# Kernel tuning notes

Measured on AMD Instinct MI355X. Metric: run time of the kernel, lower is better.

Reference implementation:

```python
import jax, jax.numpy as jnp
import numpy as np

EPS = 1e-12  # torch F.normalize eps


def setup_inputs() -> dict:
    key = jax.random.key(0)
    k1, k2, k3 = jax.random.split(key, 3)
    B, way, shot, D, H, W = 64, 5, 1, 640, 5, 5
    nq = 75
    base = jax.random.normal(k1, (B, way, shot, D, H, W), dtype=jnp.float32)
    query = jax.random.normal(k2, (B, nq, D, H, W), dtype=jnp.float32)
    r = jax.random.normal(k3, (2,), dtype=jnp.float32) * 0.1
    return {"base": base, "query": query, "r": r, "neighbor_k": 5}


def reference(base, query, r, neighbor_k):
    B, way, shot, D, H, W = base.shape
    nq = query.shape[1]
    hw = H * W

    # ---- global-cosine branch: spatial-mean descriptors ----
    base_mean = base.reshape(B, way * shot, D, hw).mean(axis=-1)   # [B, way*shot, D]
    query_mean = query.reshape(B, nq, D, hw).mean(axis=-1)         # [B, nq, D]
    bm = base_mean / jnp.maximum(jnp.linalg.norm(base_mean, axis=-1, keepdims=True), EPS)
    qm = query_mean / jnp.maximum(jnp.linalg.norm(query_mean, axis=-1, keepdims=True), EPS)
    logits = jnp.einsum('bqd,bkd->bqk', qm, bm)                    # [B, nq, way*shot]

    # ---- DN4 image-to-class branch (vectorized over the original triple loop) ----
    # query local descriptors: [B, nq, hw, D], L2-normalized over channels
    q = query.reshape(B, nq, D, hw).transpose(0, 1, 3, 2)
    q = q / jnp.linalg.norm(q, axis=-1, keepdims=True)
    # support local descriptors: base_mix [B, way, shot*D, hw], column-normalized
    s = base.reshape(B, way, shot * D, hw)
    s = s / jnp.linalg.norm(s, axis=2, keepdims=True)
    # cosine sims between every query patch and every support patch of each class
    # (requires shot*D == D, i.e. shot == 1, as in the original code)
    sim = jnp.einsum('bqpd,bkdl->bqkpl', q, s)                     # [B, nq, way, hw, hw]
    topk_vals, _ = jax.lax.top_k(sim, neighbor_k)                  # [B, nq, way, hw, k]
    logits_dn4 = topk_vals.sum(axis=(-1, -2)) / neighbor_k         # [B, nq, way]

    return r[0] * logits + r[1] * logits_dn4
```

## Files before the change

### kernel.cpp

```cpp
#include <hip/hip_runtime.h>
#include <hip/hip_bf16.h>
#include <math.h>

#define NB    64
#define WAY   5
#define DCH   640
#define HW    25
#define NQ    75
#define NBK   5
#define EPSN  1e-12f

#define QPB   4
#define BPB   ((NQ + QPB - 1) / QPB)
#define NWK   (NB * BPB)
#define NDG   (DCH / 8)
#define SCOLS 128
#define CD    32
#define NCHK  (DCH / CD)
#define CFL   (CD * HW)

typedef __attribute__((ext_vector_type(8)))  short  bf16x8;
typedef __attribute__((ext_vector_type(8)))  ushort u16x8;
typedef __attribute__((ext_vector_type(16))) float  f32x16;
typedef __attribute__((ext_vector_type(4)))  float  f32x4;

#define AS1 __attribute__((address_space(1)))
#define AS3 __attribute__((address_space(3)))

__device__ inline ushort f2bf(float f) {
    uint u = __float_as_uint(f);
    return (ushort)((u + 0x7FFFu + ((u >> 16) & 1u)) >> 16);
}

__global__ __launch_bounds__(256) void k_prep(const float* __restrict__ base,
                                              float* __restrict__ invs,
                                              float* __restrict__ invsm,
                                              ushort* __restrict__ sT)
{
    const int bk = blockIdx.x;
    const int b  = bk / WAY;
    const int k  = bk - b * WAY;
    const float* src = base + (size_t)bk * (DCH * HW);
    __shared__ float lds[DCH * HW];
    __shared__ float red[256];
    const int tid = threadIdx.x;

    const f32x4* s4 = (const f32x4*)src;
    f32x4* l4 = (f32x4*)lds;
    for (int i = tid; i < (DCH * HW) / 4; i += 256)
        l4[i] = __builtin_nontemporal_load(s4 + i);
    __syncthreads();

    if (tid < HW) {
        float ss = 0.f;
        for (int d = 0; d < DCH; ++d) { float v = lds[d * HW + tid]; ss = fmaf(v, v, ss); }
        invs[bk * HW + tid] = rsqrtf(ss);
    }

    float ssq = 0.f;
    for (int d = tid; d < DCH; d += 256) {
        float s = 0.f;
        #pragma unroll
        for (int pp = 0; pp < HW; ++pp) s += lds[d * HW + pp];
        float m = s * (1.0f / HW);
        ssq = fmaf(m, m, ssq);
    }
    red[tid] = ssq;
    __syncthreads();
    for (int s = 128; s > 0; s >>= 1) {
        if (tid < s) red[tid] += red[tid + s];
        __syncthreads();
    }
    if (tid == 0) invsm[bk] = 1.0f / fmaxf(sqrtf(red[0]), EPSN);

    ushort* dstb = sT + (size_t)b * (NDG * SCOLS * 8);
    for (int t = tid; t < NDG * HW; t += 256) {
        const int dg = t / HW, l = t - dg * HW;
        u16x8 v;
        #pragma unroll
        for (int e = 0; e < 8; ++e) v[e] = f2bf(lds[(dg * 8 + e) * HW + l]);
        *(u16x8*)&dstb[((size_t)dg * SCOLS + k * HW + l) * 8] = v;
    }
    if (k == 0) {
        const u16x8 z = (u16x8)(ushort)0;
        for (int t = tid; t < NDG * 3; t += 256) {
            const int dg = t / 3, sc = 125 + (t - dg * 3);
            *(u16x8*)&dstb[((size_t)dg * SCOLS + sc) * 8] = z;
        }
    }
}

__global__ __launch_bounds__(256, 2) void k_fused(const float* __restrict__ query,
                                                  const ushort* __restrict__ sT,
                                                  const float* __restrict__ invs,
                                                  const float* __restrict__ invsm,
                                                  const float* __restrict__ r,
                                                  float* __restrict__ out)
{
    __shared__ __align__(16) float lds_q[QPB][2][CFL];
    __shared__ float invs_l[SCOLS];
    __shared__ float invsm_l[WAY];

    const int tid  = threadIdx.x;
    const int wid  = tid >> 6;
    const int lane = tid & 63;
    const int p    = lane & 31;
    const int hi   = lane >> 5;

    const int wk = (blockIdx.x & 7) * (int)(gridDim.x >> 3) + (blockIdx.x >> 3);
    const int b  = wk / BPB;
    const int qb = wk - b * BPB;
    const int q  = qb * QPB + wid;
    const bool qok = q < NQ;

    if (tid < WAY * HW) invs_l[tid] = invs[b * WAY * HW + tid];
    if (tid >= WAY * HW && tid < SCOLS) invs_l[tid] = 0.f;
    if (tid < WAY)      invsm_l[tid] = invsm[b * WAY + tid];
    __syncthreads();
    if (!qok) return;

    f32x16 acc0 = {}, acc1 = {}, acc2 = {}, acc3 = {}, accg = {};

    const int pc = (p < HW) ? p : (HW - 1);
    const float* qrow = query + (size_t)(b * NQ + q) * (DCH * HW);
    const ushort* sTb = sT + (size_t)b * (NDG * SCOLS * 8);

#define ISSUE(c)                                                               \
    {                                                                          \
        const float* src_ = qrow + (c) * CFL;                                  \
        float* dst_ = &lds_q[wid][(c) & 1][0];                                 \
        _Pragma("unroll")                                                      \
        for (int i = 0; i < 3; ++i)                                            \
            __builtin_amdgcn_global_load_lds(                                  \
                (const AS1 uint*)(src_ + i * 256 + lane * 4),                  \
                (AS3 uint*)(dst_ + i * 256), 16, 0, 0);                        \
        if (lane < 8)                                                          \
            __builtin_amdgcn_global_load_lds(                                  \
                (const AS1 uint*)(src_ + 768 + lane * 4),                      \
                (AS3 uint*)(dst_ + 768), 16, 0, 0);                            \
    }

#define LOAD_AF(BANK, c)                                                       \
    {                                                                          \
        _Pragma("unroll")                                                      \
        for (int ks = 0; ks < 2; ++ks) {                                       \
            const int dg = (c) * 4 + ks * 2 + hi;                              \
            const bf16x8* arow = (const bf16x8*)(sTb + (size_t)dg * SCOLS * 8);\
            BANK[ks * 4 + 0] = arow[p];                                        \
            BANK[ks * 4 + 1] = arow[32 + p];                                   \
            BANK[ks * 4 + 2] = arow[64 + p];                                   \
            BANK[ks * 4 + 3] = arow[96 + p];                                   \
        }                                                                      \
    }

#define COMPUTE(c, BANK)                                                       \
    {                                                                          \
        __builtin_amdgcn_s_setprio(1);                                         \
        const float* qb_lds = &lds_q[wid][(c) & 1][hi * 8 * HW + pc];          \
        _Pragma("unroll")                                                      \
        for (int ks = 0; ks < 2; ++ks) {                                       \
            const float v0 = qb_lds[(ks * 16 + 0) * HW];                       \
            const float v1 = qb_lds[(ks * 16 + 1) * HW];                       \
            const float v2 = qb_lds[(ks * 16 + 2) * HW];                       \
            const float v3 = qb_lds[(ks * 16 + 3) * HW];                       \
            const float v4 = qb_lds[(ks * 16 + 4) * HW];                       \
            const float v5 = qb_lds[(ks * 16 + 5) * HW];                       \
            const float v6 = qb_lds[(ks * 16 + 6) * HW];                       \
            const float v7 = qb_lds[(ks * 16 + 7) * HW];                       \
            union { uint u[4]; bf16x8 v; } bqu;                                \
            asm("v_cvt_pk_bf16_f32 %0, %1, %2" : "=v"(bqu.u[0]) : "v"(v0), "v"(v1)); \
            asm("v_cvt_pk_bf16_f32 %0, %1, %2" : "=v"(bqu.u[1]) : "v"(v2), "v"(v3)); \
            asm("v_cvt_pk_bf16_f32 %0, %1, %2" : "=v"(bqu.u[2]) : "v"(v4), "v"(v5)); \
            asm("v_cvt_pk_bf16_f32 %0, %1, %2" : "=v"(bqu.u[3]) : "v"(v6), "v"(v7)); \
            const bf16x8 bq = bqu.v;                                           \
            acc0 = __builtin_amdgcn_mfma_f32_32x32x16_bf16(BANK[ks * 4 + 0], bq, acc0, 0, 0, 0); \
            acc1 = __builtin_amdgcn_mfma_f32_32x32x16_bf16(BANK[ks * 4 + 1], bq, acc1, 0, 0, 0); \
            acc2 = __builtin_amdgcn_mfma_f32_32x32x16_bf16(BANK[ks * 4 + 2], bq, acc2, 0, 0, 0); \
            acc3 = __builtin_amdgcn_mfma_f32_32x32x16_bf16(BANK[ks * 4 + 3], bq, acc3, 0, 0, 0); \
            accg = __builtin_amdgcn_mfma_f32_32x32x16_bf16(bq, bq, accg, 0, 0, 0); \
        }                                                                      \
        __builtin_amdgcn_s_setprio(0);                                         \
    }

#define STEP(c, CUR, NXT)                                                      \
    {                                                                          \
        if ((c) + 1 < NCHK) {                                                  \
            asm volatile("s_waitcnt lgkmcnt(0)" ::: "memory");                 \
            ISSUE((c) + 1)                                                     \
            LOAD_AF(NXT, (c) + 1)                                              \
            asm volatile("s_waitcnt vmcnt(12)" ::: "memory");                  \
        } else {                                                               \
            asm volatile("s_waitcnt vmcnt(0)" ::: "memory");                   \
        }                                                                      \
        __builtin_amdgcn_sched_barrier(0);                                     \
        COMPUTE(c, CUR)                                                        \
    }

    bf16x8 afA[8], afB[8];
    ISSUE(0)
    LOAD_AF(afA, 0)

    #pragma unroll 1
    for (int c = 0; c < NCHK; c += 2) {
        STEP(c,     afA, afB)
        STEP(c + 1, afB, afA)
    }
#undef ISSUE
#undef LOAD_AF
#undef COMPUTE
#undef STEP

    const bool pok = p < HW;

    float diag = 0.f, qq = 0.f;
    #pragma unroll
    for (int rr = 0; rr < 16; ++rr) {
        const int rowb = (rr & 3) + 8 * (rr >> 2);
        const int row  = rowb + 4 * hi;
        diag = (row == p) ? accg[rr] : diag;
        if (row < HW && pok) qq += accg[rr];
    }
    diag += __shfl_xor(diag, 32);
    const float invq = rsqrtf(diag);

    float gs[WAY] = {0.f, 0.f, 0.f, 0.f, 0.f};
#define TILE_SUM(ACC, T)                                            \
    _Pragma("unroll")                                               \
    for (int rr = 0; rr < 16; ++rr) {                               \
        const int s0 = (T) * 32 + (rr & 3) + 8 * (rr >> 2);         \
        const float v0 = (hi || !pok) ? 0.f : ACC[rr];              \
        const float v1 = (hi && pok) ? ACC[rr] : 0.f;               \
        if (s0 < 125)     gs[s0 / 25]       += v0;                  \
        if (s0 + 4 < 125) gs[(s0 + 4) / 25] += v1;                  \
    }
    TILE_SUM(acc0, 0) TILE_SUM(acc1, 1) TILE_SUM(acc2, 2) TILE_SUM(acc3, 3)
#undef TILE_SUM

    #pragma unroll
    for (int o = 1; o < 64; o <<= 1) {
        qq += __shfl_xor(qq, o);
        #pragma unroll
        for (int g = 0; g < WAY; ++g) gs[g] += __shfl_xor(gs[g], o);
    }

#define SCALE(ACC, T)                                               \
    _Pragma("unroll")                                               \
    for (int rr = 0; rr < 16; ++rr) {                               \
        const int s0 = (T) * 32 + (rr & 3) + 8 * (rr >> 2);         \
        ACC[rr] *= invs_l[s0 + 4 * hi];                             \
    }
    SCALE(acc0, 0) SCALE(acc1, 1) SCALE(acc2, 2) SCALE(acc3, 3)
#undef SCALE

    float tots[WAY];
    #pragma unroll
    for (int g = 0; g < WAY; ++g) {
        float t0 = -3.402823466e38f, t1 = t0, t2 = t0, t3 = t0, t4 = t0;
        #pragma unroll
        for (int j = 0; j < HW; ++j) {
            const int scol = g * HW + j;
            const int t = scol >> 5, row = scol & 31;
            const int hreq = (row >> 2) & 1;
            const int rr = (row & 3) | ((row >> 3) << 2);
            const float av = (t == 0) ? acc0[rr] : (t == 1) ? acc1[rr]
                           : (t == 2) ? acc2[rr] : acc3[rr];
            float mine = (hi == hreq) ? av : 0.f;
            mine += __shfl_xor(mine, 32);
            float x = mine, a;
            a = fmaxf(t0, x); x = fminf(t0, x); t0 = a;
            a = fmaxf(t1, x); x = fminf(t1, x); t1 = a;
            a = fmaxf(t2, x); x = fminf(t2, x); t2 = a;
            a = fmaxf(t3, x); x = fminf(t3, x); t3 = a;
            a = fmaxf(t4, x); x = fminf(t4, x); t4 = a;
        }
        tots[g] = pok ? (t0 + t1 + t2 + t3 + t4) * invq : 0.f;
    }
    #pragma unroll
    for (int o = 1; o < 64; o <<= 1) {
        #pragma unroll
        for (int g = 0; g < WAY; ++g) tots[g] += __shfl_xor(tots[g], o);
    }

    const float r0 = r[0], r1 = r[1];
    const float invqm = 1.0f / fmaxf(sqrtf(qq) * (1.0f / HW), EPSN);
    float res[WAY];
    #pragma unroll
    for (int g = 0; g < WAY; ++g)
        res[g] = r0 * gs[g] * (1.0f / 625.0f) * invqm * invsm_l[g]
               + r1 * tots[g] * 0.5f * (1.0f / NBK);

    float ov = res[0];
    ov = (lane == 1) ? res[1] : ov;
    ov = (lane == 2) ? res[2] : ov;
    ov = (lane == 3) ? res[3] : ov;
    ov = (lane == 4) ? res[4] : ov;
    if (lane < WAY) out[(size_t)(b * NQ + q) * WAY + lane] = ov;
}

extern "C" void kernel_launch(void* const* d_in, const int* in_sizes, int n_in,
                              void* d_out, int out_size, void* d_ws, size_t ws_size,
                              hipStream_t stream)
{
    const float* base  = (const float*)d_in[0];
    const float* query = (const float*)d_in[1];
    const float* r     = (const float*)d_in[2];
    float* out = (float*)d_out;

    float* invs   = (float*)d_ws;
    float* invsm  = invs + NB * WAY * HW;
    ushort* sT    = (ushort*)((float*)d_ws + 16384);

    k_prep<<<NB * WAY, 256, 0, stream>>>(base, invs, invsm, sT);
    k_fused<<<NWK, 256, 0, stream>>>(query, sT, invs, invsm, r, out);
}
```

Before: 108.0 us.

## Deepen query LDS prefetch pipeline to four stages with explicit epilogue

Grows the per-wave query staging buffer in LDS from two to four chunk slots and issues global-to-LDS loads three chunks ahead instead of one. The loop is restructured so that support-fragment loads are issued before the LDS-wait, and an explicit tail drains the remaining chunks with decreasing vmcnt thresholds. The aim is to hide global memory latency of the query stream behind MFMA work. In exchange it doubles the query LDS footprint, which may limit occupancy, and makes the vmcnt bookkeeping more fragile.

Result: no change. 108.4 us (+0.3%).

```diff
diff --git a/kernel.cpp b/kernel.cpp
--- a/kernel.cpp
+++ b/kernel.cpp
@@ -97,7 +97,7 @@
                                                   const float* __restrict__ r,
                                                   float* __restrict__ out)
 {
-    __shared__ __align__(16) float lds_q[QPB][2][CFL];
+    __shared__ __align__(16) float lds_q[QPB][4][CFL];
     __shared__ float invs_l[SCOLS];
     __shared__ float invsm_l[WAY];
 
@@ -128,7 +128,7 @@
 #define ISSUE(c)                                                               \
     {                                                                          \
         const float* src_ = qrow + (c) * CFL;                                  \
-        float* dst_ = &lds_q[wid][(c) & 1][0];                                 \
+        float* dst_ = &lds_q[wid][(c) & 3][0];                                 \
         _Pragma("unroll")                                                      \
         for (int i = 0; i < 3; ++i)                                            \
             __builtin_amdgcn_global_load_lds(                                  \
@@ -156,7 +156,7 @@
 #define COMPUTE(c, BANK)                                                       \
     {                                                                          \
         __builtin_amdgcn_s_setprio(1);                                         \
-        const float* qb_lds = &lds_q[wid][(c) & 1][hi * 8 * HW + pc];          \
+        const float* qb_lds = &lds_q[wid][(c) & 3][hi * 8 * HW + pc];          \
         _Pragma("unroll")                                                      \
         for (int ks = 0; ks < 2; ++ks) {                                       \
             const float v0 = qb_lds[(ks * 16 + 0) * HW];                       \
@@ -182,33 +182,48 @@
         __builtin_amdgcn_s_setprio(0);                                         \
     }
 
-#define STEP(c, CUR, NXT)                                                      \
-    {                                                                          \
-        if ((c) + 1 < NCHK) {                                                  \
-            asm volatile("s_waitcnt lgkmcnt(0)" ::: "memory");                 \
-            ISSUE((c) + 1)                                                     \
-            LOAD_AF(NXT, (c) + 1)                                              \
-            asm volatile("s_waitcnt vmcnt(12)" ::: "memory");                  \
-        } else {                                                               \
-            asm volatile("s_waitcnt vmcnt(0)" ::: "memory");                   \
-        }                                                                      \
+#define STEP_SS(c, CUR, NXT)                                                   \
+    {                                                                          \
+        LOAD_AF(NXT, (c) + 1)                                                  \
+        asm volatile("s_waitcnt lgkmcnt(0)" ::: "memory");                     \
+        ISSUE((c) + 3)                                                         \
+        asm volatile("s_waitcnt vmcnt(16)" ::: "memory");                      \
         __builtin_amdgcn_sched_barrier(0);                                     \
         COMPUTE(c, CUR)                                                        \
     }
 
+#define STEP_T(c, CUR, NXT, VMASM)                                             \
+    {                                                                          \
+        LOAD_AF(NXT, (c) + 1)                                                  \
+        asm volatile(VMASM ::: "memory");                                      \
+        __builtin_amdgcn_sched_barrier(0);                                     \
+        COMPUTE(c, CUR)                                                        \
+    }
+
     bf16x8 afA[8], afB[8];
-    ISSUE(0)
+    ISSUE(0) ISSUE(1)
+    __builtin_amdgcn_sched_barrier(0);
     LOAD_AF(afA, 0)
+    __builtin_amdgcn_sched_barrier(0);
+    ISSUE(2)
 
     #pragma unroll 1
-    for (int c = 0; c < NCHK; c += 2) {
-        STEP(c,     afA, afB)
-        STEP(c + 1, afB, afA)
-    }
+    for (int c = 0; c < NCHK - 4; c += 2) {
+        STEP_SS(c,     afA, afB)
+        STEP_SS(c + 1, afB, afA)
+    }
+    STEP_SS(16, afA, afB)
+    STEP_T(17, afB, afA, "s_waitcnt vmcnt(12)")
+    STEP_T(18, afA, afB, "s_waitcnt vmcnt(8)")
+    asm volatile("s_waitcnt vmcnt(0)" ::: "memory");
+    __builtin_amdgcn_sched_barrier(0);
+    COMPUTE(19, afB)
+
 #undef ISSUE
 #undef LOAD_AF
 #undef COMPUTE
-#undef STEP
+#undef STEP_SS
+#undef STEP_T
 
     const bool pok = p < HW;
 
```
